# Kernel tuning notes

Hardware: AMD Instinct MI355X
Metric: run time of the kernel (lower is better)

The kernel has to match this reference:

```python
import jax, jax.numpy as jnp
import numpy as np

EPS = 1e-5


def _segment_norm(x, seg, num_segments):
    # x: [N, D], seg: [N] sorted segment ids in [0, num_segments)
    ones = jnp.ones((x.shape[0],), x.dtype)
    cnt = jax.ops.segment_sum(ones, seg, num_segments=num_segments)      # [B]
    safe = jnp.maximum(cnt, 1.0)[:, None]                                # avoid 0-div
    mean = jax.ops.segment_sum(x, seg, num_segments=num_segments) / safe # [B, D]
    centered = x - mean[seg]
    var = jax.ops.segment_sum(centered * centered, seg, num_segments=num_segments) / safe
    std = jnp.sqrt(var)                                                  # unbiased=False
    normed = centered / (std[seg] + EPS)
    # graphs with a single element are passed through unchanged
    return jnp.where((cnt > 1.0)[seg][:, None], normed, x)


def setup_inputs() -> dict:
    key = jax.random.key(0)
    k1, k2, k3, k4 = jax.random.split(key, 4)
    N, D, B = 1_000_000, 128, 1024
    node_feat = jax.random.normal(k1, (N, D), dtype=jnp.float32)
    edge_feat = jax.random.normal(k2, (N, D), dtype=jnp.float32)
    node_seg = jnp.sort(jax.random.randint(k3, (N,), 0, B, dtype=jnp.int32))
    edge_seg = jnp.sort(jax.random.randint(k4, (N,), 0, B, dtype=jnp.int32))
    return {
        "node_feat": node_feat,
        "edge_feat": edge_feat,
        "node_gamma": jnp.ones((D,), jnp.float32),
        "node_beta": jnp.zeros((D,), jnp.float32),
        "edge_gamma": jnp.ones((D,), jnp.float32),
        "edge_beta": jnp.zeros((D,), jnp.float32),
        "node_seg": node_seg,
        "edge_seg": edge_seg,
        "num_graphs": B,
    }


def reference(node_feat, edge_feat, node_gamma, node_beta, edge_gamma, edge_beta,
              node_seg, edge_seg, num_graphs):
    node_out = _segment_norm(node_feat, node_seg, num_graphs) * node_gamma + node_beta
    edge_out = _segment_norm(edge_feat, edge_seg, num_graphs) * edge_gamma + edge_beta
    return (node_out, edge_out)
```

## Files before the change

kernel.cpp:

```cpp
#include <hip/hip_runtime.h>


static constexpr int   D4     = 32;
static constexpr int   CHUNK  = 64;
static constexpr int   NCHUNK = 4;
static constexpr int   TILE_W = CHUNK * NCHUNK;
static constexpr int   TILE_B = TILE_W * 4;
static constexpr float EPS    = 1e-5f;

typedef float vfloat4 __attribute__((ext_vector_type(4)));

#define WAITV(N) do { asm volatile("s_waitcnt vmcnt(" #N ")" ::: "memory"); \
                      __builtin_amdgcn_sched_barrier(0); } while (0)

__device__ __forceinline__ void nt_store4(float4* p, const float4& v) {
    vfloat4 w = { v.x, v.y, v.z, v.w };
    __builtin_nontemporal_store(w, reinterpret_cast<vfloat4*>(p));
}

__device__ __forceinline__ void acc4(float4& s, float4& q, const float4& v) {
    s.x += v.x; s.y += v.y; s.z += v.z; s.w += v.w;
    q.x += v.x * v.x; q.y += v.y * v.y;
    q.z += v.z * v.z; q.w += v.w * v.w;
}

__global__ __launch_bounds__(256) void seg_norm_async(
    const float4* __restrict__ xn, const float4* __restrict__ xe,
    const float*  __restrict__ gn, const float*  __restrict__ bn,
    const float*  __restrict__ ge, const float*  __restrict__ be,
    const int*    __restrict__ sn, const int*    __restrict__ se,
    float4* __restrict__ on, float4* __restrict__ oe,
    int N)
{
    __shared__ float4 stage[4][2][TILE_W];
    __shared__ float4 redS[256], redQ[256];
    __shared__ int    s_bounds[2];

    const bool is_edge = (blockIdx.y != 0);
    const float4* __restrict__ x   = is_edge ? xe : xn;
    const float*  __restrict__ gam = is_edge ? ge : gn;
    const float*  __restrict__ bet = is_edge ? be : bn;
    const int*    __restrict__ seg = is_edge ? se : sn;
    float4*       __restrict__ out = is_edge ? oe : on;

    const int b   = (int)blockIdx.x;
    const int tid = (int)threadIdx.x;

    if (tid < 2) {
        const int target = b + tid;
        int lo = 0, hi = N;
        while (lo < hi) {
            int mid = (lo + hi) >> 1;
            if (seg[mid] < target) lo = mid + 1; else hi = mid;
        }
        s_bounds[tid] = lo;
    }
    __syncthreads();
    const int start = s_bounds[0];
    const int end   = s_bounds[1];
    const int cnt   = end - start;
    if (cnt <= 0) return;

    const int w    = tid >> 6;
    const int lane = tid & 63;
    const int dg   = tid & 31;

    const size_t f4base = (size_t)start * D4;
    const int    f4cnt  = cnt * D4;
    const int    nt     = f4cnt / TILE_B;

    float4* const sb0 = &stage[w][0][0];
    float4* const sb1 = &stage[w][1][0];

    auto issue = [&](int t, float4* lp) {
        const float4* gp = x + f4base + (size_t)t * TILE_B + w * TILE_W + lane;
        #pragma unroll
        for (int i = 0; i < NCHUNK; ++i)
            __builtin_amdgcn_global_load_lds(gp + i * CHUNK, lp + i * CHUNK, 16, 0, 0);
    };

    float4 s = make_float4(0.f, 0.f, 0.f, 0.f);
    float4 q = make_float4(0.f, 0.f, 0.f, 0.f);
    if (nt > 0) {
        issue(0, sb0);
        for (int t = 0; t < nt; ++t) {
            float4* cur = (t & 1) ? sb1 : sb0;
            float4* nxt = (t & 1) ? sb0 : sb1;
            if (t + 1 < nt) { issue(t + 1, nxt); WAITV(4); }
            else            { WAITV(0); }
            #pragma unroll
            for (int i = 0; i < NCHUNK; ++i)
                acc4(s, q, cur[i * CHUNK + lane]);
        }
    }
    for (int j = nt * TILE_B + tid; j < f4cnt; j += 256)
        acc4(s, q, x[f4base + j]);

    redS[tid] = s; redQ[tid] = q;
    __syncthreads();

    if (tid < 32) {
        float4 S = redS[tid], Q = redQ[tid];
        #pragma unroll
        for (int k = 1; k < 8; ++k) {
            const float4 a = redS[k * 32 + tid];
            const float4 c = redQ[k * 32 + tid];
            S.x += a.x; S.y += a.y; S.z += a.z; S.w += a.w;
            Q.x += c.x; Q.y += c.y; Q.z += c.z; Q.w += c.w;
        }
        const float rc = 1.0f / (float)cnt;
        float4 m, iv;
        m.x = S.x * rc; m.y = S.y * rc; m.z = S.z * rc; m.w = S.w * rc;
        const float vx = fmaxf(Q.x * rc - m.x * m.x, 0.f);
        const float vy = fmaxf(Q.y * rc - m.y * m.y, 0.f);
        const float vz = fmaxf(Q.z * rc - m.z * m.z, 0.f);
        const float vw = fmaxf(Q.w * rc - m.w * m.w, 0.f);
        iv.x = 1.0f / (sqrtf(vx) + EPS);
        iv.y = 1.0f / (sqrtf(vy) + EPS);
        iv.z = 1.0f / (sqrtf(vz) + EPS);
        iv.w = 1.0f / (sqrtf(vw) + EPS);
        if (cnt <= 1) {
            m.x = m.y = m.z = m.w = 0.f;
            iv.x = iv.y = iv.z = iv.w = 1.f;
        }
        const float4 g4 = ((const float4*)gam)[tid];
        const float4 b4 = ((const float4*)bet)[tid];
        float4 A, Bc;
        A.x = iv.x * g4.x; A.y = iv.y * g4.y;
        A.z = iv.z * g4.z; A.w = iv.w * g4.w;
        Bc.x = b4.x - m.x * A.x; Bc.y = b4.y - m.y * A.y;
        Bc.z = b4.z - m.z * A.z; Bc.w = b4.w - m.w * A.w;
        redS[tid] = A; redQ[tid] = Bc;
    }
    __syncthreads();
    const float4 A  = redS[dg];
    const float4 Bc = redQ[dg];
    __syncthreads();

    if (nt > 0) {
        issue(0, sb0);
        for (int t = 0; t < nt; ++t) {
            float4* cur = (t & 1) ? sb1 : sb0;
            float4* nxt = (t & 1) ? sb0 : sb1;
            const bool hn = (t + 1 < nt);
            if (hn) issue(t + 1, nxt);
            if (t == 0) { if (hn) WAITV(4); else WAITV(0); }
            else        { if (hn) WAITV(8); else WAITV(4); }
            float4* op = out + f4base + (size_t)t * TILE_B + w * TILE_W + lane;
            #pragma unroll
            for (int i = 0; i < NCHUNK; ++i) {
                const float4 v = cur[i * CHUNK + lane];
                float4 o;
                o.x = v.x * A.x + Bc.x; o.y = v.y * A.y + Bc.y;
                o.z = v.z * A.z + Bc.z; o.w = v.w * A.w + Bc.w;
                nt_store4(op + i * CHUNK, o);
            }
        }
    }
    for (int j = nt * TILE_B + tid; j < f4cnt; j += 256) {
        const float4 v = x[f4base + j];
        float4 o;
        o.x = v.x * A.x + Bc.x; o.y = v.y * A.y + Bc.y;
        o.z = v.z * A.z + Bc.z; o.w = v.w * A.w + Bc.w;
        nt_store4(&((float4*)out)[f4base + j], o);
    }
}

extern "C" void kernel_launch(void* const* d_in, const int* in_sizes, int n_in,
                              void* d_out, int out_size, void* d_ws, size_t ws_size,
                              hipStream_t stream) {
    const float* node_feat  = (const float*)d_in[0];
    const float* edge_feat  = (const float*)d_in[1];
    const float* node_gamma = (const float*)d_in[2];
    const float* node_beta  = (const float*)d_in[3];
    const float* edge_gamma = (const float*)d_in[4];
    const float* edge_beta  = (const float*)d_in[5];
    const int*   node_seg   = (const int*)d_in[6];
    const int*   edge_seg   = (const int*)d_in[7];

    const int D = in_sizes[2];
    const int N = in_sizes[0] / D;
    const int B = 1024;

    float* out_node = (float*)d_out;
    float* out_edge = out_node + (size_t)N * (size_t)D;

    dim3 grid((unsigned)B, 2);
    seg_norm_async<<<grid, 256, 0, stream>>>(
        (const float4*)node_feat, (const float4*)edge_feat,
        node_gamma, node_beta, edge_gamma, edge_beta,
        node_seg, edge_seg,
        (float4*)out_node, (float4*)out_edge, N);
}
```

Measured before the change: 569.1 us.

## Fuse node and edge segment norms into one block with interleaved passes

Each block now handles one graph for both the node and edge tensors instead of splitting them over a 2-row grid. The node output pass is interleaved with the edge statistics pass, so both streams of loads are in flight together through the async global-to-LDS double buffering. Grid size halves to 1024 blocks and LDS staging doubles, which reduces parallelism and occupancy. In exchange, each block keeps more memory requests outstanding.

```diff
diff --git a/kernel.cpp b/kernel.cpp
--- a/kernel.cpp
+++ b/kernel.cpp
@@ -24,7 +24,15 @@
     q.z += v.z * v.z; q.w += v.w * v.w;
 }
 
-__global__ __launch_bounds__(256) void seg_norm_async(
+__device__ __forceinline__ float4 affine4(const float4& v, const float4& A,
+                                          const float4& Bc) {
+    float4 o;
+    o.x = v.x * A.x + Bc.x; o.y = v.y * A.y + Bc.y;
+    o.z = v.z * A.z + Bc.z; o.w = v.w * A.w + Bc.w;
+    return o;
+}
+
+__global__ __launch_bounds__(256) void seg_norm_fused(
     const float4* __restrict__ xn, const float4* __restrict__ xe,
     const float*  __restrict__ gn, const float*  __restrict__ bn,
     const float*  __restrict__ ge, const float*  __restrict__ be,
@@ -32,48 +40,41 @@
     float4* __restrict__ on, float4* __restrict__ oe,
     int N)
 {
-    __shared__ float4 stage[4][2][TILE_W];
+    __shared__ float4 stage[4][2][2][TILE_W];
     __shared__ float4 redS[256], redQ[256];
-    __shared__ int    s_bounds[2];
-
-    const bool is_edge = (blockIdx.y != 0);
-    const float4* __restrict__ x   = is_edge ? xe : xn;
-    const float*  __restrict__ gam = is_edge ? ge : gn;
-    const float*  __restrict__ bet = is_edge ? be : bn;
-    const int*    __restrict__ seg = is_edge ? se : sn;
-    float4*       __restrict__ out = is_edge ? oe : on;
-
-    const int b   = (int)blockIdx.x;
-    const int tid = (int)threadIdx.x;
-
-    if (tid < 2) {
-        const int target = b + tid;
+    __shared__ int    sb[4];
+
+    const int b    = (int)blockIdx.x;
+    const int tid  = (int)threadIdx.x;
+    const int w    = tid >> 6;
+    const int lane = tid & 63;
+    const int dg   = tid & 31;
+
+    if (tid < 4) {
+        const int* sg    = (tid < 2) ? sn : se;
+        const int target = b + (tid & 1);
         int lo = 0, hi = N;
         while (lo < hi) {
             int mid = (lo + hi) >> 1;
-            if (seg[mid] < target) lo = mid + 1; else hi = mid;
-        }
-        s_bounds[tid] = lo;
-    }
-    __syncthreads();
-    const int start = s_bounds[0];
-    const int end   = s_bounds[1];
-    const int cnt   = end - start;
-    if (cnt <= 0) return;
-
-    const int w    = tid >> 6;
-    const int lane = tid & 63;
-    const int dg   = tid & 31;
-
-    const size_t f4base = (size_t)start * D4;
-    const int    f4cnt  = cnt * D4;
-    const int    nt     = f4cnt / TILE_B;
-
-    float4* const sb0 = &stage[w][0][0];
-    float4* const sb1 = &stage[w][1][0];
-
-    auto issue = [&](int t, float4* lp) {
-        const float4* gp = x + f4base + (size_t)t * TILE_B + w * TILE_W + lane;
+            if (sg[mid] < target) lo = mid + 1; else hi = mid;
+        }
+        sb[tid] = lo;
+    }
+    __syncthreads();
+    const int    stN = sb[0], cntN = sb[1] - sb[0];
+    const int    stE = sb[2], cntE = sb[3] - sb[2];
+    const size_t fbN = (size_t)stN * D4;  const int fcN = cntN * D4;
+    const size_t fbE = (size_t)stE * D4;  const int fcE = cntE * D4;
+    const int    ntN = fcN / TILE_B,      ntE = fcE / TILE_B;
+    const int    tmid = min(ntN, ntE);
+
+    float4* const nb0 = &stage[w][0][0][0];
+    float4* const nb1 = &stage[w][0][1][0];
+    float4* const eb0 = &stage[w][1][0][0];
+    float4* const eb1 = &stage[w][1][1][0];
+
+    auto issue = [&](const float4* src, size_t fb, int t, float4* lp) {
+        const float4* gp = src + fb + (size_t)t * TILE_B + w * TILE_W + lane;
         #pragma unroll
         for (int i = 0; i < NCHUNK; ++i)
             __builtin_amdgcn_global_load_lds(gp + i * CHUNK, lp + i * CHUNK, 16, 0, 0);
@@ -81,89 +82,128 @@
 
     float4 s = make_float4(0.f, 0.f, 0.f, 0.f);
     float4 q = make_float4(0.f, 0.f, 0.f, 0.f);
-    if (nt > 0) {
-        issue(0, sb0);
-        for (int t = 0; t < nt; ++t) {
-            float4* cur = (t & 1) ? sb1 : sb0;
-            float4* nxt = (t & 1) ? sb0 : sb1;
-            if (t + 1 < nt) { issue(t + 1, nxt); WAITV(4); }
-            else            { WAITV(0); }
+    if (ntN > 0) {
+        issue(xn, fbN, 0, nb0);
+        for (int t = 0; t < ntN; ++t) {
+            float4* cur = (t & 1) ? nb1 : nb0;
+            float4* nxt = (t & 1) ? nb0 : nb1;
+            if (t + 1 < ntN) { issue(xn, fbN, t + 1, nxt); WAITV(4); }
+            else             { WAITV(0); }
             #pragma unroll
             for (int i = 0; i < NCHUNK; ++i)
                 acc4(s, q, cur[i * CHUNK + lane]);
         }
     }
-    for (int j = nt * TILE_B + tid; j < f4cnt; j += 256)
-        acc4(s, q, x[f4base + j]);
+    for (int j = ntN * TILE_B + tid; j < fcN; j += 256)
+        acc4(s, q, xn[fbN + j]);
 
     redS[tid] = s; redQ[tid] = q;
     __syncthreads();
-
     if (tid < 32) {
         float4 S = redS[tid], Q = redQ[tid];
         #pragma unroll
         for (int k = 1; k < 8; ++k) {
-            const float4 a = redS[k * 32 + tid];
-            const float4 c = redQ[k * 32 + tid];
+            const float4 a = redS[k * 32 + tid], c = redQ[k * 32 + tid];
             S.x += a.x; S.y += a.y; S.z += a.z; S.w += a.w;
             Q.x += c.x; Q.y += c.y; Q.z += c.z; Q.w += c.w;
         }
-        const float rc = 1.0f / (float)cnt;
+        const float rc = 1.0f / (float)max(cntN, 1);
         float4 m, iv;
         m.x = S.x * rc; m.y = S.y * rc; m.z = S.z * rc; m.w = S.w * rc;
-        const float vx = fmaxf(Q.x * rc - m.x * m.x, 0.f);
-        const float vy = fmaxf(Q.y * rc - m.y * m.y, 0.f);
-        const float vz = fmaxf(Q.z * rc - m.z * m.z, 0.f);
-        const float vw = fmaxf(Q.w * rc - m.w * m.w, 0.f);
-        iv.x = 1.0f / (sqrtf(vx) + EPS);
-        iv.y = 1.0f / (sqrtf(vy) + EPS);
-        iv.z = 1.0f / (sqrtf(vz) + EPS);
-        iv.w = 1.0f / (sqrtf(vw) + EPS);
-        if (cnt <= 1) {
-            m.x = m.y = m.z = m.w = 0.f;
-            iv.x = iv.y = iv.z = iv.w = 1.f;
-        }
-        const float4 g4 = ((const float4*)gam)[tid];
-        const float4 b4 = ((const float4*)bet)[tid];
+        iv.x = 1.0f / (sqrtf(fmaxf(Q.x * rc - m.x * m.x, 0.f)) + EPS);
+        iv.y = 1.0f / (sqrtf(fmaxf(Q.y * rc - m.y * m.y, 0.f)) + EPS);
+        iv.z = 1.0f / (sqrtf(fmaxf(Q.z * rc - m.z * m.z, 0.f)) + EPS);
+        iv.w = 1.0f / (sqrtf(fmaxf(Q.w * rc - m.w * m.w, 0.f)) + EPS);
+        if (cntN <= 1) { m = make_float4(0,0,0,0); iv = make_float4(1,1,1,1); }
+        const float4 g4 = ((const float4*)gn)[tid];
+        const float4 b4 = ((const float4*)bn)[tid];
         float4 A, Bc;
-        A.x = iv.x * g4.x; A.y = iv.y * g4.y;
-        A.z = iv.z * g4.z; A.w = iv.w * g4.w;
+        A.x = iv.x * g4.x; A.y = iv.y * g4.y; A.z = iv.z * g4.z; A.w = iv.w * g4.w;
         Bc.x = b4.x - m.x * A.x; Bc.y = b4.y - m.y * A.y;
         Bc.z = b4.z - m.z * A.z; Bc.w = b4.w - m.w * A.w;
         redS[tid] = A; redQ[tid] = Bc;
     }
     __syncthreads();
-    const float4 A  = redS[dg];
-    const float4 Bc = redQ[dg];
-    __syncthreads();
-
-    if (nt > 0) {
-        issue(0, sb0);
-        for (int t = 0; t < nt; ++t) {
-            float4* cur = (t & 1) ? sb1 : sb0;
-            float4* nxt = (t & 1) ? sb0 : sb1;
-            const bool hn = (t + 1 < nt);
-            if (hn) issue(t + 1, nxt);
+    const float4 A0  = redS[dg];
+    const float4 Bc0 = redQ[dg];
+    __syncthreads();
+
+    s = make_float4(0.f, 0.f, 0.f, 0.f);
+    q = make_float4(0.f, 0.f, 0.f, 0.f);
+    if (tmid > 0) {
+        issue(xe, fbE, 0, eb0);
+        issue(xn, fbN, 0, nb0);
+        for (int t = 0; t < tmid; ++t) {
+            float4* ecur = (t & 1) ? eb1 : eb0;
+            float4* enxt = (t & 1) ? eb0 : eb1;
+            float4* ncur = (t & 1) ? nb1 : nb0;
+            float4* nnxt = (t & 1) ? nb0 : nb1;
+            const bool hn = (t + 1 < tmid);
+            if (hn) { issue(xe, fbE, t + 1, enxt); issue(xn, fbN, t + 1, nnxt); }
+            if (t == 0) { if (hn) WAITV(8);  else WAITV(0); }
+            else        { if (hn) WAITV(12); else WAITV(4); }
+            float4* op = on + fbN + (size_t)t * TILE_B + w * TILE_W + lane;
+            #pragma unroll
+            for (int i = 0; i < NCHUNK; ++i) {
+                acc4(s, q, ecur[i * CHUNK + lane]);
+                nt_store4(op + i * CHUNK, affine4(ncur[i * CHUNK + lane], A0, Bc0));
+            }
+        }
+        WAITV(0);
+    }
+    for (int j = tmid * TILE_B + tid; j < fcN; j += 256)
+        nt_store4(&on[fbN + j], affine4(xn[fbN + j], A0, Bc0));
+    for (int j = tmid * TILE_B + tid; j < fcE; j += 256)
+        acc4(s, q, xe[fbE + j]);
+
+    __syncthreads();
+    redS[tid] = s; redQ[tid] = q;
+    __syncthreads();
+    if (tid < 32) {
+        float4 S = redS[tid], Q = redQ[tid];
+        #pragma unroll
+        for (int k = 1; k < 8; ++k) {
+            const float4 a = redS[k * 32 + tid], c = redQ[k * 32 + tid];
+            S.x += a.x; S.y += a.y; S.z += a.z; S.w += a.w;
+            Q.x += c.x; Q.y += c.y; Q.z += c.z; Q.w += c.w;
+        }
+        const float rc = 1.0f / (float)max(cntE, 1);
+        float4 m, iv;
+        m.x = S.x * rc; m.y = S.y * rc; m.z = S.z * rc; m.w = S.w * rc;
+        iv.x = 1.0f / (sqrtf(fmaxf(Q.x * rc - m.x * m.x, 0.f)) + EPS);
+        iv.y = 1.0f / (sqrtf(fmaxf(Q.y * rc - m.y * m.y, 0.f)) + EPS);
+        iv.z = 1.0f / (sqrtf(fmaxf(Q.z * rc - m.z * m.z, 0.f)) + EPS);
+        iv.w = 1.0f / (sqrtf(fmaxf(Q.w * rc - m.w * m.w, 0.f)) + EPS);
+        if (cntE <= 1) { m = make_float4(0,0,0,0); iv = make_float4(1,1,1,1); }
+        const float4 g4 = ((const float4*)ge)[tid];
+        const float4 b4 = ((const float4*)be)[tid];
+        float4 A, Bc;
+        A.x = iv.x * g4.x; A.y = iv.y * g4.y; A.z = iv.z * g4.z; A.w = iv.w * g4.w;
+        Bc.x = b4.x - m.x * A.x; Bc.y = b4.y - m.y * A.y;
+        Bc.z = b4.z - m.z * A.z; Bc.w = b4.w - m.w * A.w;
+        redS[tid] = A; redQ[tid] = Bc;
+    }
+    __syncthreads();
+    const float4 A1  = redS[dg];
+    const float4 Bc1 = redQ[dg];
+
+    if (ntE > 0) {
+        issue(xe, fbE, 0, eb0);
+        for (int t = 0; t < ntE; ++t) {
+            float4* cur = (t & 1) ? eb1 : eb0;
+            float4* nxt = (t & 1) ? eb0 : eb1;
+            const bool hn = (t + 1 < ntE);
+            if (hn) issue(xe, fbE, t + 1, nxt);
             if (t == 0) { if (hn) WAITV(4); else WAITV(0); }
             else        { if (hn) WAITV(8); else WAITV(4); }
-            float4* op = out + f4base + (size_t)t * TILE_B + w * TILE_W + lane;
+            float4* op = oe + fbE + (size_t)t * TILE_B + w * TILE_W + lane;
             #pragma unroll
-            for (int i = 0; i < NCHUNK; ++i) {
-                const float4 v = cur[i * CHUNK + lane];
-                float4 o;
-                o.x = v.x * A.x + Bc.x; o.y = v.y * A.y + Bc.y;
-                o.z = v.z * A.z + Bc.z; o.w = v.w * A.w + Bc.w;
-                nt_store4(op + i * CHUNK, o);
-            }
-        }
-    }
-    for (int j = nt * TILE_B + tid; j < f4cnt; j += 256) {
-        const float4 v = x[f4base + j];
-        float4 o;
-        o.x = v.x * A.x + Bc.x; o.y = v.y * A.y + Bc.y;
-        o.z = v.z * A.z + Bc.z; o.w = v.w * A.w + Bc.w;
-        nt_store4(&((float4*)out)[f4base + j], o);
-    }
+            for (int i = 0; i < NCHUNK; ++i)
+                nt_store4(op + i * CHUNK, affine4(cur[i * CHUNK + lane], A1, Bc1));
+        }
+    }
+    for (int j = ntE * TILE_B + tid; j < fcE; j += 256)
+        nt_store4(&oe[fbE + j], affine4(xe[fbE + j], A1, Bc1));
 }
 
 extern "C" void kernel_launch(void* const* d_in, const int* in_sizes, int n_in,
@@ -185,8 +225,7 @@
     float* out_node = (float*)d_out;
     float* out_edge = out_node + (size_t)N * (size_t)D;
 
-    dim3 grid((unsigned)B, 2);
-    seg_norm_async<<<grid, 256, 0, stream>>>(
+    seg_norm_fused<<<dim3((unsigned)B), 256, 0, stream>>>(
         (const float4*)node_feat, (const float4*)edge_feat,
         node_gamma, node_beta, edge_gamma, edge_beta,
         node_seg, edge_seg,
```

Result: faster. 555.9 us (-2.3%).
